# Kernel optimization log

Measured on AMD Instinct MI355X. Metric: run time of the kernel, lower is better.

Reference implementation:

```python
import jax, jax.numpy as jnp
import numpy as np

NEG_SLOPE = 0.2  # PyG GATConv leaky_relu slope


def _add_self_loops(edge_index, num_nodes):
    loops = jnp.arange(num_nodes, dtype=edge_index.dtype)
    src = jnp.concatenate([edge_index[0], loops])
    dst = jnp.concatenate([edge_index[1], loops])
    return src, dst


def _gat_conv(x, src, dst, W, a_src, a_dst, b, num_nodes):
    # W: [in, H*F]; a_src, a_dst: [H, F]; b: [H*F]
    H, F = a_src.shape
    h = (x @ W).reshape(num_nodes, H, F)                # [N,H,F]
    alpha_src = jnp.einsum('nhf,hf->nh', h, a_src)      # [N,H]
    alpha_dst = jnp.einsum('nhf,hf->nh', h, a_dst)      # [N,H]
    logits = alpha_src[src] + alpha_dst[dst]            # [E,H]
    logits = jax.nn.leaky_relu(logits, NEG_SLOPE)
    # segment softmax over incoming edges of each dst node
    seg_max = jax.ops.segment_max(logits, dst, num_segments=num_nodes)  # [N,H]
    e = jnp.exp(logits - seg_max[dst])                  # [E,H]
    denom = jax.ops.segment_sum(e, dst, num_segments=num_nodes)         # [N,H]
    alpha = e / denom[dst]                              # [E,H] (self-loops guarantee denom>0)
    msg = h[src] * alpha[:, :, None]                    # [E,H,F]
    out = jax.ops.segment_sum(msg, dst, num_segments=num_nodes)         # [N,H,F]
    return out.reshape(num_nodes, H * F) + b            # concat=True


def _gcn_conv(x, src, dst, W, b, num_nodes):
    h = x @ W                                           # [N,out]
    ones = jnp.ones(dst.shape[0], dtype=h.dtype)
    deg = jax.ops.segment_sum(ones, dst, num_segments=num_nodes)        # [N]
    dinv = jnp.where(deg > 0, jax.lax.rsqrt(deg), 0.0)
    norm = dinv[src] * dinv[dst]                        # [E]
    out = jax.ops.segment_sum(h[src] * norm[:, None], dst, num_segments=num_nodes)
    return out + b


def setup_inputs() -> dict:
    key = jax.random.key(0)
    ks = jax.random.split(key, 10)
    N, E = 50000, 800000
    in_dim, hid, H1, ncls = 128, 32, 8, 16
    s = 0.05
    d = {}
    d['x'] = jax.random.normal(ks[0], (N, in_dim), jnp.float32)
    d['edge_index'] = jax.random.randint(ks[1], (2, E), 0, N)
    # GATConv 1: in=128 -> hid=32, heads=8
    d['W1'] = jax.random.normal(ks[2], (in_dim, H1 * hid), jnp.float32) * s
    d['a_src1'] = jax.random.normal(ks[3], (H1, hid), jnp.float32) * s
    d['a_dst1'] = jax.random.normal(ks[4], (H1, hid), jnp.float32) * s
    d['b1'] = jnp.zeros((H1 * hid,), jnp.float32)
    # GATConv 2: in=256 -> hid//2=16, heads=1
    d['W2'] = jax.random.normal(ks[5], (H1 * hid, hid // 2), jnp.float32) * s
    d['a_src2'] = jax.random.normal(ks[6], (1, hid // 2), jnp.float32) * s
    d['a_dst2'] = jax.random.normal(ks[7], (1, hid // 2), jnp.float32) * s
    d['b2'] = jnp.zeros((hid // 2,), jnp.float32)
    # GCNConv: 16 -> 16 classes
    d['W3'] = jax.random.normal(ks[8], (hid // 2, ncls), jnp.float32) * s
    d['b3'] = jnp.zeros((ncls,), jnp.float32)
    return d


def reference(x, edge_index, W1, a_src1, a_dst1, b1, W2, a_src2, a_dst2, b2, W3, b3):
    N = x.shape[0]
    src, dst = _add_self_loops(edge_index, N)
    # dropout layers are identity in eval mode
    h = _gat_conv(x, src, dst, W1, a_src1, a_dst1, b1, N)
    h = jax.nn.elu(h)
    h = _gat_conv(h, src, dst, W2, a_src2, a_dst2, b2, N)
    h = jax.nn.elu(h)
    out = _gcn_conv(h, src, dst, W3, b3, N)
    return out
```

## Files before the change

kernel.cpp:

```cpp
#include <hip/hip_runtime.h>
#include <hip/hip_bf16.h>
#include <math.h>

#define NEG_SLOPE 0.2f
#define DEG_CAP 64
#define FPAD 16

typedef float f32x4 __attribute__((ext_vector_type(4)));
typedef short bf16x8 __attribute__((ext_vector_type(8)));
typedef unsigned int u32x2 __attribute__((ext_vector_type(2)));

static __device__ __forceinline__ float lrelu(float x) { return x > 0.f ? x : NEG_SLOPE * x; }
static __device__ __forceinline__ float elu1(float x)  { return x > 0.f ? x : (expf(x) - 1.f); }

static __device__ __forceinline__ unsigned short f2bf(float x) {
    __hip_bfloat16 h = __float2bfloat16(x);
    return *reinterpret_cast<unsigned short*>(&h);
}
static __device__ __forceinline__ unsigned int pack2bf(float a, float b) {
    return (unsigned int)f2bf(a) | ((unsigned int)f2bf(b) << 16);
}
static __device__ __forceinline__ float bflo(unsigned int u) { return __uint_as_float(u << 16); }
static __device__ __forceinline__ float bfhi(unsigned int u) { return __uint_as_float(u & 0xFFFF0000u); }

__global__ __launch_bounds__(256) void init_kernel(int* __restrict__ fillc_p, const float* __restrict__ W1,
                                                   unsigned short* __restrict__ Wb, int N) {
    int i = blockIdx.x * 256 + threadIdx.x;
    if (i < N) fillc_p[i * FPAD] = 0;
    if (i < 32768) {
        int j = i & 7, lane = (i >> 3) & 63, t = (i >> 9) & 15, kk = i >> 13;
        int k = kk * 32 + (lane >> 4) * 8 + j;
        int n = t * 16 + (lane & 15);
        Wb[i] = f2bf(W1[k * 256 + n]);
    }
}

__global__ __launch_bounds__(256) void fill_kernel(const int* __restrict__ ei, int* __restrict__ fillc_p,
                                                   int* __restrict__ srcs_p, int E, int E2) {
    int g = blockIdx.x & 7;
    int i = (blockIdx.x >> 3) * 256 + threadIdx.x;
    if (i >= E2) return;
    int src, dst;
    if (i < E) { src = ei[i]; dst = ei[E + i]; }
    else       { src = i - E; dst = i - E; }
    if ((dst & 7) != g) return;
    int pos = atomicAdd(&fillc_p[(size_t)dst * FPAD], 1);
    if (pos < DEG_CAP) srcs_p[(size_t)dst * DEG_CAP + pos] = src;
}

__global__ __launch_bounds__(256) void gemm1_kernel(const float* __restrict__ x, const unsigned short* __restrict__ Wb,
                                                    const float* __restrict__ a_src, const float* __restrict__ a_dst,
                                                    unsigned short* __restrict__ h1b, float* __restrict__ as1,
                                                    float* __restrict__ ad1, int M) {
    int w = threadIdx.x >> 6, lane = threadIdx.x & 63;
    int quad = lane >> 4, c = lane & 15;
    int rowA = blockIdx.x * 64 + w * 16 + c;
    int rowAc = rowA < M ? rowA : M - 1;
    f32x4 acc[16];
    #pragma unroll
    for (int t = 0; t < 16; t++) acc[t] = (f32x4){0.f, 0.f, 0.f, 0.f};
    #pragma unroll
    for (int kk = 0; kk < 4; kk++) {
        const float* ap = &x[(size_t)rowAc * 128 + kk * 32 + quad * 8];
        float4 a0 = *(const float4*)ap;
        float4 a1 = *(const float4*)(ap + 4);
        union { bf16x8 v; unsigned int u[4]; } af;
        af.u[0] = pack2bf(a0.x, a0.y); af.u[1] = pack2bf(a0.z, a0.w);
        af.u[2] = pack2bf(a1.x, a1.y); af.u[3] = pack2bf(a1.z, a1.w);
        const bf16x8* bp = (const bf16x8*)&Wb[(size_t)(kk * 16) * 512 + lane * 8];
        #pragma unroll
        for (int t = 0; t < 16; t++) {
            bf16x8 bf = bp[t * 64];
            acc[t] = __builtin_amdgcn_mfma_f32_16x16x32_bf16(af.v, bf, acc[t], 0, 0, 0);
        }
    }
    int growb = blockIdx.x * 64 + w * 16 + quad * 4;
    #pragma unroll
    for (int r = 0; r < 4; r++) {
        int grow = growb + r;
        if (grow < M) {
            #pragma unroll
            for (int t = 0; t < 16; t++)
                h1b[(size_t)grow * 256 + t * 16 + c] = f2bf(acc[t][r]);
        }
    }
    float asA[8], asB[8], adA[8], adB[8];
    #pragma unroll
    for (int h = 0; h < 8; h++) {
        asA[h] = a_src[h * 32 + c];      asB[h] = a_src[h * 32 + 16 + c];
        adA[h] = a_dst[h * 32 + c];      adB[h] = a_dst[h * 32 + 16 + c];
    }
    #pragma unroll
    for (int r = 0; r < 4; r++) {
        int grow = growb + r;
        #pragma unroll
        for (int h = 0; h < 8; h++) {
            float ps = acc[2 * h][r] * asA[h] + acc[2 * h + 1][r] * asB[h];
            float pd = acc[2 * h][r] * adA[h] + acc[2 * h + 1][r] * adB[h];
            ps += __shfl_xor(ps, 1); ps += __shfl_xor(ps, 2); ps += __shfl_xor(ps, 4); ps += __shfl_xor(ps, 8);
            pd += __shfl_xor(pd, 1); pd += __shfl_xor(pd, 2); pd += __shfl_xor(pd, 4); pd += __shfl_xor(pd, 8);
            if (c == 0 && grow < M) { as1[grow * 8 + h] = ps; ad1[grow * 8 + h] = pd; }
        }
    }
}

__global__ __launch_bounds__(256) void agg1_kernel(const unsigned short* __restrict__ h1b, const float* __restrict__ asrc,
                                                   const float* __restrict__ adst, const int* __restrict__ fillc_p,
                                                   const int* __restrict__ srcs_p, const float* __restrict__ b1,
                                                   unsigned short* __restrict__ h1pb, int n0, int n1) {
    int node = n0 + blockIdx.x * 4 + (threadIdx.x >> 6);
    if (node >= n1) return;
    int lane = threadIdx.x & 63;
    int h = lane >> 3, e8 = lane & 7;
    float adn = adst[node * 8 + h];
    int deg = fillc_p[(size_t)node * FPAD];
    int cnt = deg < DEG_CAP ? deg : DEG_CAP;
    float4 acc = make_float4(0.f, 0.f, 0.f, 0.f);
    float den = 0.f;
    int o4 = lane * 4;
    int sv = srcs_p[node * DEG_CAP + (lane < cnt ? lane : cnt - 1)];
    int g = 0;
    for (; g + 16 <= cnt; g += 16) {
        int ssA = __shfl(sv, g + e8);
        int ssB = __shfl(sv, g + 8 + e8);
        float wA = __expf(lrelu(asrc[ssA * 8 + h] + adn));
        float wB = __expf(lrelu(asrc[ssB * 8 + h] + adn));
        uint2 v[16];
        #pragma unroll
        for (int q = 0; q < 16; q++) {
            int s = __shfl(sv, g + q);
            v[q] = *(const uint2*)&h1b[(size_t)s * 256 + o4];
        }
        #pragma unroll
        for (int q = 0; q < 8; q++) {
            float w = __shfl(wA, (h << 3) | q);
            acc.x += w * bflo(v[q].x); acc.y += w * bfhi(v[q].x);
            acc.z += w * bflo(v[q].y); acc.w += w * bfhi(v[q].y);
            den += w;
        }
        #pragma unroll
        for (int q = 8; q < 16; q++) {
            float w = __shfl(wB, (h << 3) | (q - 8));
            acc.x += w * bflo(v[q].x); acc.y += w * bfhi(v[q].x);
            acc.z += w * bflo(v[q].y); acc.w += w * bfhi(v[q].y);
            den += w;
        }
    }
    if (g + 8 <= cnt) {
        int ss = __shfl(sv, g + e8);
        float wp = __expf(lrelu(asrc[ss * 8 + h] + adn));
        uint2 v[8];
        #pragma unroll
        for (int q = 0; q < 8; q++) {
            int s = __shfl(sv, g + q);
            v[q] = *(const uint2*)&h1b[(size_t)s * 256 + o4];
        }
        #pragma unroll
        for (int q = 0; q < 8; q++) {
            float w = __shfl(wp, (h << 3) | q);
            acc.x += w * bflo(v[q].x); acc.y += w * bfhi(v[q].x);
            acc.z += w * bflo(v[q].y); acc.w += w * bfhi(v[q].y);
            den += w;
        }
        g += 8;
    }
    if (g < cnt) {
        int ep = g + e8;
        int epc = ep < cnt - 1 ? ep : cnt - 1;
        int ss = __shfl(sv, epc);
        float wp = (ep < cnt) ? __expf(lrelu(asrc[ss * 8 + h] + adn)) : 0.f;
        #pragma unroll
        for (int q = 0; q < 8; q++) {
            if (g + q < cnt) {
                int s = __shfl(sv, g + q);
                float w = __shfl(wp, (h << 3) | q);
                uint2 vv = *(const uint2*)&h1b[(size_t)s * 256 + o4];
                acc.x += w * bflo(vv.x); acc.y += w * bfhi(vv.x);
                acc.z += w * bflo(vv.y); acc.w += w * bfhi(vv.y);
                den += w;
            }
        }
    }
    float inv = 1.f / den;
    u32x2 r;
    r.x = pack2bf(elu1(acc.x * inv + b1[o4 + 0]), elu1(acc.y * inv + b1[o4 + 1]));
    r.y = pack2bf(elu1(acc.z * inv + b1[o4 + 2]), elu1(acc.w * inv + b1[o4 + 3]));
    __builtin_nontemporal_store(r, (u32x2*)&h1pb[(size_t)node * 256 + o4]);
}

__global__ __launch_bounds__(256) void gemm2_kernel(const unsigned short* __restrict__ X, const float* __restrict__ W2,
                                                    const float* __restrict__ a_src2, const float* __restrict__ a_dst2,
                                                    const int* __restrict__ fillc_p, float* __restrict__ h2,
                                                    float* __restrict__ asrc2, float* __restrict__ adst2,
                                                    float* __restrict__ dinv, int N) {
    int lane = threadIdx.x & 63;
    int c = lane & 15, kq = lane >> 4;
    int wid = blockIdx.x * (blockDim.x >> 6) + (threadIdx.x >> 6);
    int nwaves = gridDim.x * (blockDim.x >> 6);
    float w2r[64];
    #pragma unroll
    for (int i = 0; i < 64; i++) w2r[i] = W2[(kq * 64 + i) * 16 + c];
    float as_c = a_src2[c], ad_c = a_dst2[c];
    for (int n = wid; n < N; n += nwaves) {
        const unsigned short* xp = &X[(size_t)n * 256 + kq * 64];
        float acc = 0.f;
        #pragma unroll
        for (int i8 = 0; i8 < 8; i8++) {
            uint4 xv = *(const uint4*)&xp[i8 * 8];
            int b = i8 * 8;
            acc += bflo(xv.x) * w2r[b+0] + bfhi(xv.x) * w2r[b+1]
                 + bflo(xv.y) * w2r[b+2] + bfhi(xv.y) * w2r[b+3]
                 + bflo(xv.z) * w2r[b+4] + bfhi(xv.z) * w2r[b+5]
                 + bflo(xv.w) * w2r[b+6] + bfhi(xv.w) * w2r[b+7];
        }
        acc += __shfl_xor(acc, 16);
        acc += __shfl_xor(acc, 32);
        float s1 = acc * as_c, s2 = acc * ad_c;
        #pragma unroll
        for (int off = 1; off < 16; off <<= 1) { s1 += __shfl_xor(s1, off); s2 += __shfl_xor(s2, off); }
        if (kq == 0) h2[n * 16 + c] = acc;
        if (lane == 0) {
            asrc2[n] = s1; adst2[n] = s2;
            dinv[n] = rsqrtf((float)fillc_p[(size_t)n * FPAD]);
        }
    }
}

__global__ __launch_bounds__(256) void agg2_kernel(const float* __restrict__ h2, const float* __restrict__ asrc2,
                                                   const float* __restrict__ adst2, const int* __restrict__ fillc_p,
                                                   const int* __restrict__ srcs_p, const float* __restrict__ b2,
                                                   const float* __restrict__ W3, float* __restrict__ h4, int N) {
    int node = blockIdx.x * 4 + (threadIdx.x >> 6);
    if (node >= N) return;
    int lane = threadIdx.x & 63;
    int e16 = lane >> 2, seg = lane & 3;
    float adn = adst2[node];
    int deg = fillc_p[(size_t)node * FPAD];
    int cnt = deg < DEG_CAP ? deg : DEG_CAP;
    int sv = srcs_p[node * DEG_CAP + (lane < cnt ? lane : cnt - 1)];
    float wv = (lane < cnt) ? __expf(lrelu(asrc2[sv] + adn)) : 0.f;
    float w[4]; float4 v[4];
    #pragma unroll
    for (int r = 0; r < 4; r++) {
        int j = r * 16 + e16;
        int s = __shfl(sv, j);
        w[r] = __shfl(wv, j);
        v[r] = *(const float4*)&h2[(size_t)s * 16 + seg * 4];
    }
    float4 acc = make_float4(0.f, 0.f, 0.f, 0.f);
    float den = 0.f;
    #pragma unroll
    for (int r = 0; r < 4; r++) {
        acc.x += w[r] * v[r].x; acc.y += w[r] * v[r].y;
        acc.z += w[r] * v[r].z; acc.w += w[r] * v[r].w;
        den += w[r];
    }
    #pragma unroll
    for (int off = 4; off < 64; off <<= 1) {
        acc.x += __shfl_xor(acc.x, off); acc.y += __shfl_xor(acc.y, off);
        acc.z += __shfl_xor(acc.z, off); acc.w += __shfl_xor(acc.w, off);
        den += __shfl_xor(den, off);
    }
    float inv = 1.f / den;
    float h3v[4];
    h3v[0] = elu1(acc.x * inv + b2[seg * 4 + 0]);
    h3v[1] = elu1(acc.y * inv + b2[seg * 4 + 1]);
    h3v[2] = elu1(acc.z * inv + b2[seg * 4 + 2]);
    h3v[3] = elu1(acc.w * inv + b2[seg * 4 + 3]);
    int c = lane & 15;
    float h4v = 0.f;
    #pragma unroll
    for (int cs = 0; cs < 16; cs++) {
        float hv = __shfl(h3v[cs & 3], cs >> 2);
        h4v += hv * W3[cs * 16 + c];
    }
    if (lane < 16) h4[node * 16 + c] = h4v;
}

__global__ __launch_bounds__(256) void agg3_kernel(const float* __restrict__ h4, const float* __restrict__ dinv,
                                                   const int* __restrict__ fillc_p, const int* __restrict__ srcs_p,
                                                   const float* __restrict__ b3, float* __restrict__ out, int N) {
    int node = blockIdx.x * 4 + (threadIdx.x >> 6);
    if (node >= N) return;
    int lane = threadIdx.x & 63;
    int e16 = lane >> 2, seg = lane & 3;
    int deg = fillc_p[(size_t)node * FPAD];
    int cnt = deg < DEG_CAP ? deg : DEG_CAP;
    int sv = srcs_p[node * DEG_CAP + (lane < cnt ? lane : cnt - 1)];
    float wv = (lane < cnt) ? dinv[sv] : 0.f;
    float w[4]; float4 v[4];
    #pragma unroll
    for (int r = 0; r < 4; r++) {
        int j = r * 16 + e16;
        int s = __shfl(sv, j);
        w[r] = __shfl(wv, j);
        v[r] = *(const float4*)&h4[(size_t)s * 16 + seg * 4];
    }
    float4 acc = make_float4(0.f, 0.f, 0.f, 0.f);
    #pragma unroll
    for (int r = 0; r < 4; r++) {
        acc.x += w[r] * v[r].x; acc.y += w[r] * v[r].y;
        acc.z += w[r] * v[r].z; acc.w += w[r] * v[r].w;
    }
    #pragma unroll
    for (int off = 4; off < 64; off <<= 1) {
        acc.x += __shfl_xor(acc.x, off); acc.y += __shfl_xor(acc.y, off);
        acc.z += __shfl_xor(acc.z, off); acc.w += __shfl_xor(acc.w, off);
    }
    if (lane < 4) {
        float dn = dinv[node];
        float4 r;
        r.x = acc.x * dn + b3[seg * 4 + 0];
        r.y = acc.y * dn + b3[seg * 4 + 1];
        r.z = acc.z * dn + b3[seg * 4 + 2];
        r.w = acc.w * dn + b3[seg * 4 + 3];
        *(float4*)&out[(size_t)node * 16 + seg * 4] = r;
    }
}

extern "C" void kernel_launch(void* const* d_in, const int* in_sizes, int n_in,
                              void* d_out, int out_size, void* d_ws, size_t ws_size,
                              hipStream_t stream) {
    const float* x      = (const float*)d_in[0];
    const int*   ei     = (const int*)d_in[1];
    const float* W1     = (const float*)d_in[2];
    const float* a_src1 = (const float*)d_in[3];
    const float* a_dst1 = (const float*)d_in[4];
    const float* b1     = (const float*)d_in[5];
    const float* W2     = (const float*)d_in[6];
    const float* a_src2 = (const float*)d_in[7];
    const float* a_dst2 = (const float*)d_in[8];
    const float* b2     = (const float*)d_in[9];
    const float* W3     = (const float*)d_in[10];
    const float* b3     = (const float*)d_in[11];
    float* out = (float*)d_out;

    const int N  = in_sizes[0] / 128;
    const int E  = in_sizes[1] / 2;
    const int E2 = E + N;

    char* p = (char*)d_ws;
    auto alloc = [&](size_t bytes) -> void* {
        void* r = (void*)p;
        p += (bytes + 255) & ~(size_t)255;
        return r;
    };
    int*   fillc_p = (int*)alloc((size_t)N * FPAD * 4);
    int*   srcs_p  = (int*)alloc((size_t)N * DEG_CAP * 4);
    unsigned short* Wb   = (unsigned short*)alloc((size_t)32768 * 2);
    unsigned short* h1b  = (unsigned short*)alloc((size_t)N * 256 * 2);
    unsigned short* h1pb = (unsigned short*)alloc((size_t)N * 256 * 2);
    float* as1    = (float*)alloc((size_t)N * 8 * 4);
    float* ad1    = (float*)alloc((size_t)N * 8 * 4);
    float* h2     = (float*)alloc((size_t)N * 16 * 4);
    float* as2    = (float*)alloc((size_t)N * 4);
    float* ad2    = (float*)alloc((size_t)N * 4);
    float* h4     = (float*)alloc((size_t)N * 16 * 4);
    float* dinv   = (float*)alloc((size_t)N * 4);

    init_kernel<<<(N + 255) / 256, 256, 0, stream>>>(fillc_p, W1, Wb, N);
    fill_kernel<<<8 * ((E2 + 255) / 256), 256, 0, stream>>>(ei, fillc_p, srcs_p, E, E2);

    gemm1_kernel<<<(N + 63) / 64, 256, 0, stream>>>(x, Wb, a_src1, a_dst1, h1b, as1, ad1, N);

    int half = N / 2;
    agg1_kernel<<<(half + 3) / 4, 256, 0, stream>>>(h1b, as1, ad1, fillc_p, srcs_p, b1, h1pb, 0, half);
    agg1_kernel<<<(N - half + 3) / 4, 256, 0, stream>>>(h1b, as1, ad1, fillc_p, srcs_p, b1, h1pb, half, N);

    gemm2_kernel<<<1024, 256, 0, stream>>>(h1pb, W2, a_src2, a_dst2, fillc_p, h2, as2, ad2, dinv, N);
    agg2_kernel<<<(N + 3) / 4, 256, 0, stream>>>(h2, as2, ad2, fillc_p, srcs_p, b2, W3, h4, N);

    agg3_kernel<<<(N + 3) / 4, 256, 0, stream>>>(h4, dinv, fillc_p, srcs_p, b3, out, N);
}
```

Measured before the change: 309.3 us.

## Pre-convert x to bf16 in init and split gemm1 columns across waves

```diff
diff --git a/kernel.cpp b/kernel.cpp
--- a/kernel.cpp
+++ b/kernel.cpp
@@ -24,14 +24,24 @@
 static __device__ __forceinline__ float bfhi(unsigned int u) { return __uint_as_float(u & 0xFFFF0000u); }
 
 __global__ __launch_bounds__(256) void init_kernel(int* __restrict__ fillc_p, const float* __restrict__ W1,
-                                                   unsigned short* __restrict__ Wb, int N) {
-    int i = blockIdx.x * 256 + threadIdx.x;
-    if (i < N) fillc_p[i * FPAD] = 0;
-    if (i < 32768) {
+                                                   unsigned short* __restrict__ Wb, const float* __restrict__ x,
+                                                   unsigned short* __restrict__ xb, int N) {
+    int gid = blockIdx.x * 256 + threadIdx.x;
+    int nth = gridDim.x * 256;
+    for (int i = gid; i < N; i += nth) fillc_p[(size_t)i * FPAD] = 0;
+    for (int i = gid; i < 32768; i += nth) {
         int j = i & 7, lane = (i >> 3) & 63, t = (i >> 9) & 15, kk = i >> 13;
         int k = kk * 32 + (lane >> 4) * 8 + j;
         int n = t * 16 + (lane & 15);
         Wb[i] = f2bf(W1[k * 256 + n]);
+    }
+    int nf4 = N * 32;
+    for (int i = gid; i < nf4; i += nth) {
+        float4 v = ((const float4*)x)[i];
+        u32x2 o;
+        o.x = pack2bf(v.x, v.y);
+        o.y = pack2bf(v.z, v.w);
+        ((u32x2*)xb)[i] = o;
     }
 }
 
@@ -48,58 +58,60 @@
     if (pos < DEG_CAP) srcs_p[(size_t)dst * DEG_CAP + pos] = src;
 }
 
-__global__ __launch_bounds__(256) void gemm1_kernel(const float* __restrict__ x, const unsigned short* __restrict__ Wb,
+__global__ __launch_bounds__(256) void gemm1_kernel(const unsigned short* __restrict__ xb,
+                                                    const unsigned short* __restrict__ Wb,
                                                     const float* __restrict__ a_src, const float* __restrict__ a_dst,
                                                     unsigned short* __restrict__ h1b, float* __restrict__ as1,
                                                     float* __restrict__ ad1, int M) {
     int w = threadIdx.x >> 6, lane = threadIdx.x & 63;
     int quad = lane >> 4, c = lane & 15;
-    int rowA = blockIdx.x * 64 + w * 16 + c;
+    int rowg = w & 1, colh = w >> 1;
+    int row0 = blockIdx.x * 32 + rowg * 16;
+    int rowA = row0 + c;
     int rowAc = rowA < M ? rowA : M - 1;
-    f32x4 acc[16];
-    #pragma unroll
-    for (int t = 0; t < 16; t++) acc[t] = (f32x4){0.f, 0.f, 0.f, 0.f};
+    f32x4 acc[8];
+    #pragma unroll
+    for (int t = 0; t < 8; t++) acc[t] = (f32x4){0.f, 0.f, 0.f, 0.f};
     #pragma unroll
     for (int kk = 0; kk < 4; kk++) {
-        const float* ap = &x[(size_t)rowAc * 128 + kk * 32 + quad * 8];
-        float4 a0 = *(const float4*)ap;
-        float4 a1 = *(const float4*)(ap + 4);
-        union { bf16x8 v; unsigned int u[4]; } af;
-        af.u[0] = pack2bf(a0.x, a0.y); af.u[1] = pack2bf(a0.z, a0.w);
-        af.u[2] = pack2bf(a1.x, a1.y); af.u[3] = pack2bf(a1.z, a1.w);
-        const bf16x8* bp = (const bf16x8*)&Wb[(size_t)(kk * 16) * 512 + lane * 8];
-        #pragma unroll
-        for (int t = 0; t < 16; t++) {
+        bf16x8 av = *(const bf16x8*)&xb[(size_t)rowAc * 128 + kk * 32 + quad * 8];
+        const bf16x8* bp = (const bf16x8*)&Wb[((size_t)(kk * 16 + colh * 8) * 64 + lane) * 8];
+        #pragma unroll
+        for (int t = 0; t < 8; t++) {
             bf16x8 bf = bp[t * 64];
-            acc[t] = __builtin_amdgcn_mfma_f32_16x16x32_bf16(af.v, bf, acc[t], 0, 0, 0);
-        }
-    }
-    int growb = blockIdx.x * 64 + w * 16 + quad * 4;
+            acc[t] = __builtin_amdgcn_mfma_f32_16x16x32_bf16(av, bf, acc[t], 0, 0, 0);
+        }
+    }
+    int growb = row0 + quad * 4;
     #pragma unroll
     for (int r = 0; r < 4; r++) {
         int grow = growb + r;
         if (grow < M) {
             #pragma unroll
-            for (int t = 0; t < 16; t++)
-                h1b[(size_t)grow * 256 + t * 16 + c] = f2bf(acc[t][r]);
-        }
-    }
-    float asA[8], asB[8], adA[8], adB[8];
-    #pragma unroll
-    for (int h = 0; h < 8; h++) {
-        asA[h] = a_src[h * 32 + c];      asB[h] = a_src[h * 32 + 16 + c];
-        adA[h] = a_dst[h * 32 + c];      adB[h] = a_dst[h * 32 + 16 + c];
+            for (int t = 0; t < 8; t++)
+                h1b[(size_t)grow * 256 + (colh * 8 + t) * 16 + c] = f2bf(acc[t][r]);
+        }
+    }
+    float asA[4], asB[4], adA[4], adB[4];
+    #pragma unroll
+    for (int hp = 0; hp < 4; hp++) {
+        int h = colh * 4 + hp;
+        asA[hp] = a_src[h * 32 + c];      asB[hp] = a_src[h * 32 + 16 + c];
+        adA[hp] = a_dst[h * 32 + c];      adB[hp] = a_dst[h * 32 + 16 + c];
     }
     #pragma unroll
     for (int r = 0; r < 4; r++) {
         int grow = growb + r;
         #pragma unroll
-        for (int h = 0; h < 8; h++) {
-            float ps = acc[2 * h][r] * asA[h] + acc[2 * h + 1][r] * asB[h];
-            float pd = acc[2 * h][r] * adA[h] + acc[2 * h + 1][r] * adB[h];
+        for (int hp = 0; hp < 4; hp++) {
+            float ps = acc[2 * hp][r] * asA[hp] + acc[2 * hp + 1][r] * asB[hp];
+            float pd = acc[2 * hp][r] * adA[hp] + acc[2 * hp + 1][r] * adB[hp];
             ps += __shfl_xor(ps, 1); ps += __shfl_xor(ps, 2); ps += __shfl_xor(ps, 4); ps += __shfl_xor(ps, 8);
             pd += __shfl_xor(pd, 1); pd += __shfl_xor(pd, 2); pd += __shfl_xor(pd, 4); pd += __shfl_xor(pd, 8);
-            if (c == 0 && grow < M) { as1[grow * 8 + h] = ps; ad1[grow * 8 + h] = pd; }
+            if (c == 0 && grow < M) {
+                int h = colh * 4 + hp;
+                as1[grow * 8 + h] = ps; ad1[grow * 8 + h] = pd;
+            }
         }
     }
 }
@@ -348,6 +360,7 @@
     int*   fillc_p = (int*)alloc((size_t)N * FPAD * 4);
     int*   srcs_p  = (int*)alloc((size_t)N * DEG_CAP * 4);
     unsigned short* Wb   = (unsigned short*)alloc((size_t)32768 * 2);
+    unsigned short* xb   = (unsigned short*)alloc((size_t)N * 128 * 2);
     unsigned short* h1b  = (unsigned short*)alloc((size_t)N * 256 * 2);
     unsigned short* h1pb = (unsigned short*)alloc((size_t)N * 256 * 2);
     float* as1    = (float*)alloc((size_t)N * 8 * 4);
@@ -358,10 +371,10 @@
     float* h4     = (float*)alloc((size_t)N * 16 * 4);
     float* dinv   = (float*)alloc((size_t)N * 4);
 
-    init_kernel<<<(N + 255) / 256, 256, 0, stream>>>(fillc_p, W1, Wb, N);
+    init_kernel<<<2048, 256, 0, stream>>>(fillc_p, W1, Wb, x, xb, N);
     fill_kernel<<<8 * ((E2 + 255) / 256), 256, 0, stream>>>(ei, fillc_p, srcs_p, E, E2);
 
-    gemm1_kernel<<<(N + 63) / 64, 256, 0, stream>>>(x, Wb, a_src1, a_dst1, h1b, as1, ad1, N);
+    gemm1_kernel<<<(N + 31) / 32, 256, 0, stream>>>(xb, Wb, a_src1, a_dst1, h1b, as1, ad1, N);
 
     int half = N / 2;
     agg1_kernel<<<(half + 3) / 4, 256, 0, stream>>>(h1b, as1, ad1, fillc_p, srcs_p, b1, h1pb, 0, half);
```

New measurement: 304.5 us. About the same (-1.5%).
